# Kernel tuning notes

Hardware: AMD Instinct MI355X
Metric: run time of the kernel (lower is better)

The kernel has to match this reference:

```python
import jax, jax.numpy as jnp
import numpy as np

N, E, DIN, H, HEADS = 50000, 800000, 128, 64, 4


def setup_inputs() -> dict:
    key = jax.random.key(0)
    ks = jax.random.split(key, 12)

    def p(k, shape, fan_in):
        return jax.random.normal(k, shape, dtype=jnp.float32) / np.float32(np.sqrt(fan_in))

    return dict(
        x=jax.random.normal(ks[0], (N, DIN), dtype=jnp.float32),
        edge_index=jax.random.randint(ks[1], (2, E), 0, N, dtype=jnp.int32),
        # GCNConv(input_dim, hidden)
        W_gcn=p(ks[2], (DIN, H), DIN), b_gcn=jnp.zeros((H,), jnp.float32),
        # GATConv(hidden, hidden, heads=4, concat=True)
        W_gat=p(ks[3], (H, HEADS * H), H),
        att_src=p(ks[4], (HEADS, H), H), att_dst=p(ks[5], (HEADS, H), H),
        b_gat=jnp.zeros((HEADS * H,), jnp.float32),
        # SAGEConv(4*hidden, hidden): lin_l (neighbors, with bias), lin_r (root, no bias)
        W_sage_l=p(ks[6], (HEADS * H, H), HEADS * H), b_sage=jnp.zeros((H,), jnp.float32),
        W_sage_r=p(ks[7], (HEADS * H, H), HEADS * H),
        # edge-pair MLP: Linear(2*hidden, hidden) -> ReLU -> Linear(hidden, 1)
        W1=p(ks[8], (2 * H, H), 2 * H), b1=jnp.zeros((H,), jnp.float32),
        W2=p(ks[9], (H, 1), H), b2=jnp.zeros((1,), jnp.float32),
    )


def reference(x, edge_index, W_gcn, b_gcn, W_gat, att_src, att_dst, b_gat,
              W_sage_l, b_sage, W_sage_r, W1, b1, W2, b2):
    n = x.shape[0]
    src, dst = edge_index[0], edge_index[1]
    loop = jnp.arange(n, dtype=edge_index.dtype)
    # edges with self-loops appended (GCN and GAT add self-loops by default)
    s2 = jnp.concatenate([src, loop])
    d2 = jnp.concatenate([dst, loop])

    h = x @ W_gcn                                            # [N, H]
    deg = jax.ops.segment_sum(jnp.ones_like(d2, jnp.float32), d2, num_segments=n)
    dinv = jnp.where(deg > 0, jax.lax.rsqrt(jnp.maximum(deg, 1e-12)), 0.0)
    norm = dinv[s2] * dinv[d2]                               # [E+N]
    h = jax.ops.segment_sum(h[s2] * norm[:, None], d2, num_segments=n) + b_gcn
    h = jax.nn.relu(h)                                       # dropout: identity in eval

    # ---- GATConv (heads=4, concat=True, negative_slope=0.2) ----
    g = (h @ W_gat).reshape(n, HEADS, H)                     # [N, heads, C]
    a_s = jnp.sum(g * att_src, axis=-1)                      # [N, heads]
    a_d = jnp.sum(g * att_dst, axis=-1)
    e = jax.nn.leaky_relu(a_s[s2] + a_d[d2], 0.2)            # [E+N, heads]
    m = jax.ops.segment_max(e, d2, num_segments=n)           # per-target max (stable softmax)
    e = jnp.exp(e - m[d2])
    z = jax.ops.segment_sum(e, d2, num_segments=n)
    alpha = e / (z[d2] + 1e-16)                              # edge softmax over incoming edges
    g = jax.ops.segment_sum(g[s2] * alpha[:, :, None], d2, num_segments=n)
    g = jax.nn.relu(g.reshape(n, HEADS * H) + b_gat)

    # ---- SAGEConv (mean aggregation, root weight, no self-loops) ----
    nsum = jax.ops.segment_sum(g[src], dst, num_segments=n)
    cnt = jax.ops.segment_sum(jnp.ones_like(dst, jnp.float32), dst, num_segments=n)
    mean = nsum / jnp.maximum(cnt, 1.0)[:, None]
    s = jax.nn.relu(mean @ W_sage_l + b_sage + g @ W_sage_r)  # [N, H]

    # ---- edge-pair MLP + sigmoid ----
    ef = jnp.concatenate([s[src], s[dst]], axis=1)            # [E, 2H]
    pred = jax.nn.relu(ef @ W1 + b1) @ W2 + b2                # [E, 1]
    return jax.nn.sigmoid(pred[:, 0])
```

## Files before the change

kernel.cpp:

```cpp
#include <hip/hip_runtime.h>
#include <math.h>

typedef float v2f __attribute__((ext_vector_type(2)));
static __device__ __forceinline__ float4 f4s(float v){ return make_float4(v,v,v,v); }
static __device__ __forceinline__ float4 f4add(float4 a, float4 b){ return make_float4(a.x+b.x,a.y+b.y,a.z+b.z,a.w+b.w); }
static __device__ __forceinline__ float4 f4max(float4 a, float4 b){ return make_float4(fmaxf(a.x,b.x),fmaxf(a.y,b.y),fmaxf(a.z,b.z),fmaxf(a.w,b.w)); }
static __device__ __forceinline__ float4 f4scale(float4 a, float s){ return make_float4(a.x*s,a.y*s,a.z*s,a.w*s); }
static __device__ __forceinline__ float4 f4fma(float4 acc, float s, float4 b){
  acc.x += s*b.x; acc.y += s*b.y; acc.z += s*b.z; acc.w += s*b.w; return acc;
}
static __device__ __forceinline__ float4 f4relu(float4 a){ return f4max(a, f4s(0.f)); }
static __device__ __forceinline__ float4 f4leaky(float4 a){
  return make_float4(a.x>0.f?a.x:0.2f*a.x, a.y>0.f?a.y:0.2f*a.y, a.z>0.f?a.z:0.2f*a.z, a.w>0.f?a.w:0.2f*a.w);
}
static __device__ __forceinline__ float4 f4expf(float4 a){ return make_float4(__expf(a.x),__expf(a.y),__expf(a.z),__expf(a.w)); }
static __device__ __forceinline__ unsigned short f2bf(float f){
  unsigned int u = __float_as_uint(f);
  unsigned int r = (u + 0x7fffu + ((u >> 16) & 1u)) >> 16;
  return (unsigned short)r;
}
static __device__ __forceinline__ ushort4 f2bf4(float4 f){
  ushort4 r; r.x=f2bf(f.x); r.y=f2bf(f.y); r.z=f2bf(f.z); r.w=f2bf(f.w); return r;
}
static __device__ __forceinline__ float4 bfu2f4(uint2 u){
  return make_float4(__uint_as_float(u.x << 16), __uint_as_float(u.x & 0xffff0000u),
                     __uint_as_float(u.y << 16), __uint_as_float(u.y & 0xffff0000u));
}
static __device__ __forceinline__ float4 bfu2f4_lo(uint4 u){ return bfu2f4(make_uint2(u.x, u.y)); }
static __device__ __forceinline__ float4 bfu2f4_hi(uint4 u){ return bfu2f4(make_uint2(u.z, u.w)); }

typedef __attribute__((ext_vector_type(8))) unsigned short u16x8;
static __device__ __forceinline__ u16x8 f2bf8(float4 a, float4 b){
  u16x8 r;
  r[0]=f2bf(a.x); r[1]=f2bf(a.y); r[2]=f2bf(a.z); r[3]=f2bf(a.w);
  r[4]=f2bf(b.x); r[5]=f2bf(b.y); r[6]=f2bf(b.z); r[7]=f2bf(b.w);
  return r;
}
static __device__ __forceinline__ void red2(float4& a, float4& b){
  a.x += __shfl_xor(a.x, 8); a.y += __shfl_xor(a.y, 8);
  a.z += __shfl_xor(a.z, 8); a.w += __shfl_xor(a.w, 8);
  b.x += __shfl_xor(b.x, 8); b.y += __shfl_xor(b.y, 8);
  b.z += __shfl_xor(b.z, 8); b.w += __shfl_xor(b.w, 8);
}
static __device__ __forceinline__ unsigned char f2fp8(float v){
  return (unsigned char)(__builtin_amdgcn_cvt_pk_fp8_f32(v, v, 0, false) & 0xff);
}
static __device__ __forceinline__ unsigned int f4_fp8x4(float4 v){
  unsigned int r = __builtin_amdgcn_cvt_pk_fp8_f32(v.x, v.y, 0, false);
  r = __builtin_amdgcn_cvt_pk_fp8_f32(v.z, v.w, r, true);
  return r;
}
static __device__ __forceinline__ float4 fp8x4_f4(unsigned int q){
  v2f lo = __builtin_amdgcn_cvt_pk_f32_fp8(q, false);
  v2f hi = __builtin_amdgcn_cvt_pk_f32_fp8(q, true);
  return make_float4(lo[0], lo[1], hi[0], hi[1]);
}
static __device__ __forceinline__ float dot8(float4 a, float4 b, const float* v){
  return a.x*v[0]+a.y*v[1]+a.z*v[2]+a.w*v[3]+b.x*v[4]+b.y*v[5]+b.z*v[6]+b.w*v[7];
}

typedef __attribute__((ext_vector_type(8))) short bf16x8;
typedef __attribute__((ext_vector_type(4))) float f32x4;

__global__ __launch_bounds__(256) void k_rank(const int* __restrict__ dst, int* __restrict__ cnt,
                                              int* __restrict__ rank, int E){
  int t = blockIdx.x*256 + threadIdx.x;
  if (t < E) rank[t] = atomicAdd(&cnt[dst[t]], 1);
}
__global__ __launch_bounds__(256) void k_scan1(const int* __restrict__ cnt, int* __restrict__ excl,
                                               int* __restrict__ bsum, int n){
  __shared__ int sc[256];
  int t = threadIdx.x; int i = blockIdx.x*256 + t;
  int v = (i<n)?cnt[i]:0;
  sc[t]=v; __syncthreads();
  for (int o=1;o<256;o<<=1){ int a=(t>=o)?sc[t-o]:0; __syncthreads(); sc[t]+=a; __syncthreads(); }
  if (i<n) excl[i] = sc[t]-v;
  if (t==255) bsum[blockIdx.x] = sc[t];
}
__global__ __launch_bounds__(256) void k_scan2v(int* __restrict__ bsum, int nb,
                                                const float* __restrict__ Wg, const float* __restrict__ as,
                                                const float* __restrict__ ad, float* __restrict__ Vs,
                                                float* __restrict__ Vd){
  __shared__ int sc[256];
  int t = threadIdx.x;
  int v = (t<nb)?bsum[t]:0;
  sc[t]=v; __syncthreads();
  for (int o=1;o<256;o<<=1){ int a=(t>=o)?sc[t-o]:0; __syncthreads(); sc[t]+=a; __syncthreads(); }
  if (t<nb) bsum[t] = sc[t]-v;
  int h = t >> 6, k = t & 63;
  float s = 0.f, d = 0.f;
  const float* wr = Wg + (size_t)k*256 + h*64;
  const float* ar = as + h*64;
  const float* dr = ad + h*64;
  for (int c = 0; c < 64; ++c){ float w = wr[c]; s += w*ar[c]; d += w*dr[c]; }
  Vs[t] = s; Vd[t] = d;
}
__global__ __launch_bounds__(256) void k_scan3(const int* __restrict__ cnt, const int* __restrict__ excl,
                                               const int* __restrict__ bsum, int* __restrict__ offs,
                                               float* __restrict__ dinv, int n, int E){
  int i = blockIdx.x*256 + threadIdx.x;
  if (i < n){
    int o = excl[i] + bsum[blockIdx.x];
    offs[i] = o;
    dinv[i] = rsqrtf((float)cnt[i] + 1.0f);
    if (i == 0) offs[n] = E;
  }
}
__global__ __launch_bounds__(256) void k_fill(const int* __restrict__ src, const int* __restrict__ dst,
                                              const int* __restrict__ offs, const int* __restrict__ rank,
                                              int* __restrict__ csr, int E){
  int t = blockIdx.x*256 + threadIdx.x;
  if (t < E) csr[offs[dst[t]] + rank[t]] = src[t];
}

template<int K, int Cout, bool IBF16, bool SCALE, bool DUAL, bool H4, bool BRELU, bool OB16, bool O8>
__global__ __launch_bounds__(256) void k_mgemm(const void* __restrict__ in, int ldin,
                                               const float* __restrict__ Wa, int ldwa,
                                               const float* __restrict__ Wb, int ldwb,
                                               unsigned short* __restrict__ out,
                                               unsigned char* __restrict__ out8, int ldout,
                                               int n, const float* __restrict__ rowscale,
                                               const float* __restrict__ bias){
  constexpr int CC = Cout >> 4;
  constexpr int KB = K >> 5;
  constexpr int NH = H4 ? 4 : 1;
  extern __shared__ unsigned short wb[];
  int tid = threadIdx.x;
  constexpr int nslots = KB*CC*64;
  for (int s = tid; s < nslots; s += 256){
    int l = s & 63;
    int f = s >> 6;
    int cc = f % CC, kb = f / CC;
    int c  = cc*16 + (l & 15);
    int kr = kb*32 + ((l >> 4) << 3);
    const float* wp; int ld;
    if (DUAL && c >= (Cout/2)){ wp = Wb + (size_t)kr*ldwb + (c - Cout/2); ld = ldwb; }
    else                      { wp = Wa + (size_t)kr*ldwa + c;            ld = ldwa; }
    unsigned short* dp = &wb[s*8];
    #pragma unroll
    for (int j = 0; j < 8; ++j) dp[j] = f2bf(wp[(size_t)j*ld]);
  }
  __syncthreads();
  int wv = tid >> 6, l = tid & 63;
  int lrow = l & 15;
  int lk = (l >> 4) << 3;
  int ngrp = (n + 63) >> 6;
  const unsigned short* inb = (const unsigned short*)in;
  const float* inf = (const float*)in;
  for (int g = blockIdx.x; g < ngrp; g += gridDim.x){
    int r0 = (g << 6) + (wv << 4);
    int m = r0 + lrow;
    bf16x8 afr[NH][KB];
    #pragma unroll
    for (int h = 0; h < NH; ++h){
      #pragma unroll
      for (int kb = 0; kb < KB; ++kb){
        bf16x8 a = {0,0,0,0,0,0,0,0};
        if (m < n){
          int off = (H4 ? h*64 : 0) + kb*32 + lk;
          if (IBF16){
            a = *(const bf16x8*)(inb + (size_t)m*ldin + off);
          } else {
            const float* p = inf + (size_t)m*ldin + off;
            float4 f0 = *(const float4*)p;
            float4 f1 = *(const float4*)(p + 4);
            a[0]=(short)f2bf(f0.x); a[1]=(short)f2bf(f0.y); a[2]=(short)f2bf(f0.z); a[3]=(short)f2bf(f0.w);
            a[4]=(short)f2bf(f1.x); a[5]=(short)f2bf(f1.y); a[6]=(short)f2bf(f1.z); a[7]=(short)f2bf(f1.w);
          }
        }
        afr[h][kb] = a;
      }
    }
    int rbase = r0 + ((l >> 4) << 2);
    float sc[4];
    if (SCALE){
      #pragma unroll
      for (int r = 0; r < 4; ++r) sc[r] = (rbase + r < n) ? rowscale[rbase + r] : 0.f;
    }
    #pragma unroll
    for (int cc = 0; cc < CC; ++cc){
      f32x4 acc = {0.f, 0.f, 0.f, 0.f};
      constexpr int hstep = H4 ? 1 : 0;
      int hh = hstep ? (cc >> 2) : 0;
      #pragma unroll
      for (int kb = 0; kb < KB; ++kb){
        bf16x8 b = *(const bf16x8*)&wb[((kb*CC + cc)*64 + l)*8];
        acc = __builtin_amdgcn_mfma_f32_16x16x32_bf16(afr[hh][kb], b, acc, 0, 0, 0);
      }
      int c = cc*16 + lrow;
      float bv = BRELU ? bias[c] : 0.f;
      #pragma unroll
      for (int r = 0; r < 4; ++r){
        int rr = rbase + r;
        if (rr < n){
          float v = acc[r];
          if (SCALE) v *= sc[r];
          if (BRELU) v = fmaxf(v + bv, 0.f);
          if (OB16) out[(size_t)rr*ldout + c] = f2bf(v);
          if (O8)   out8[(size_t)rr*ldout + c] = f2fp8(v);
        }
      }
    }
  }
}

__global__ __launch_bounds__(256) void k_gatsage(const unsigned short* __restrict__ Y,
                                                 const float* __restrict__ Wg,
                                                 const float* __restrict__ bg,
                                                 const float* __restrict__ Wl,
                                                 const float* __restrict__ Wr,
                                                 unsigned short* __restrict__ R,
                                                 unsigned char* __restrict__ P8, int n){
  constexpr int LDG = 264;
  extern __shared__ unsigned short lds[];
  unsigned short* wb1 = lds;
  unsigned short* wb2 = wb1 + 2048*8;
  unsigned short* gb  = wb2 + 4096*8;
  int tid = threadIdx.x;
  for (int s = tid; s < 2048; s += 256){
    int l = s & 63, f = s >> 6;
    int cc = f & 15, kb = f >> 4;
    int c  = cc*16 + (l & 15);
    int kr = kb*32 + ((l >> 4) << 3);
    const float* wp = Wg + (size_t)kr*256 + c;
    unsigned short* dp = &wb1[s*8];
    #pragma unroll
    for (int j = 0; j < 8; ++j) dp[j] = f2bf(wp[(size_t)j*256]);
  }
  for (int s = tid; s < 4096; s += 256){
    int l = s & 63, f = s >> 6;
    int cc = f & 7, kb = f >> 3;
    int c  = cc*16 + (l & 15);
    int kr = kb*32 + ((l >> 4) << 3);
    const float* wp = (c >= 64) ? (Wr + (size_t)kr*64 + (c - 64)) : (Wl + (size_t)kr*64 + c);
    unsigned short* dp = &wb2[s*8];
    #pragma unroll
    for (int j = 0; j < 8; ++j) dp[j] = f2bf(wp[(size_t)j*64]);
  }
  __syncthreads();
  int wv = tid >> 6, l = tid & 63;
  int lrow = l & 15;
  int lk = (l >> 4) << 3;
  int rbase4 = (l >> 4) << 2;
  int ngrp = (n + 63) >> 6;
  for (int g = blockIdx.x; g < ngrp; g += gridDim.x){
    int r0 = (g << 6) + (wv << 4);
    int m = r0 + lrow;
    bf16x8 afr[4][2];
    #pragma unroll
    for (int h = 0; h < 4; ++h){
      #pragma unroll
      for (int kb = 0; kb < 2; ++kb){
        bf16x8 a = {0,0,0,0,0,0,0,0};
        if (m < n) a = *(const bf16x8*)(Y + (size_t)m*256 + h*64 + kb*32 + lk);
        afr[h][kb] = a;
      }
    }
    #pragma unroll
    for (int cc = 0; cc < 16; ++cc){
      f32x4 acc = {0.f, 0.f, 0.f, 0.f};
      int hh = cc >> 2;
      #pragma unroll
      for (int kb = 0; kb < 2; ++kb){
        bf16x8 b = *(const bf16x8*)&wb1[((kb*16 + cc)*64 + l)*8];
        acc = __builtin_amdgcn_mfma_f32_16x16x32_bf16(afr[hh][kb], b, acc, 0, 0, 0);
      }
      int c = cc*16 + lrow;
      float bv = bg[c];
      #pragma unroll
      for (int r = 0; r < 4; ++r){
        int lr = (wv << 4) + rbase4 + r;
        gb[lr*LDG + c] = f2bf(fmaxf(acc[r] + bv, 0.f));
      }
    }
    bf16x8 afb[8];
    #pragma unroll
    for (int kb = 0; kb < 8; ++kb)
      afb[kb] = *(const bf16x8*)&gb[((wv << 4) + lrow)*LDG + kb*32 + lk];
    #pragma unroll
    for (int cc = 0; cc < 8; ++cc){
      f32x4 acc = {0.f, 0.f, 0.f, 0.f};
      #pragma unroll
      for (int kb = 0; kb < 8; ++kb){
        bf16x8 b = *(const bf16x8*)&wb2[((kb*8 + cc)*64 + l)*8];
        acc = __builtin_amdgcn_mfma_f32_16x16x32_bf16(afb[kb], b, acc, 0, 0, 0);
      }
      int c = cc*16 + lrow;
      #pragma unroll
      for (int r = 0; r < 4; ++r){
        int rr = r0 + rbase4 + r;
        if (rr < n){
          float v = acc[r];
          if (c < 64) P8[(size_t)rr*64 + c] = f2fp8(v);
          else        R[(size_t)rr*64 + (c - 64)] = f2bf(v);
        }
      }
    }
  }
}

__global__ __launch_bounds__(256) void k_gcn(const unsigned char* __restrict__ a8, const float* __restrict__ dinv,
                                             const float* __restrict__ b, const int* __restrict__ offs,
                                             const int* __restrict__ csr, const float* __restrict__ Vs,
                                             const float* __restrict__ Vd, unsigned char* __restrict__ h8,
                                             float* __restrict__ D, int n){
  __shared__ float svs[256], svd[256];
  svs[threadIdx.x] = Vs[threadIdx.x];
  svd[threadIdx.x] = Vd[threadIdx.x];
  __syncthreads();
  int l = threadIdx.x & 63;
  int node = (((blockIdx.x*256 + threadIdx.x) >> 6) << 2) + (l >> 4);
  int l15 = l & 15;
  int grp = l15 >> 3, sub = l15 & 7;
  bool ok = node < n;
  int beg = 0, end = 0;
  float di = 0.f;
  if (ok){ beg = offs[node]; end = offs[node+1]; di = dinv[node]; }
  float4 aL0 = f4s(0.f), aH0 = f4s(0.f), aL1 = f4s(0.f), aH1 = f4s(0.f);
  int i = beg + grp;
  for (; i + 2 < end; i += 4){
    int s0 = csr[i], s1 = csr[i+2];
    uint2 u0 = *(const uint2*)(a8 + (size_t)s0*64 + (sub<<3));
    uint2 u1 = *(const uint2*)(a8 + (size_t)s1*64 + (sub<<3));
    aL0 = f4add(aL0, fp8x4_f4(u0.x)); aH0 = f4add(aH0, fp8x4_f4(u0.y));
    aL1 = f4add(aL1, fp8x4_f4(u1.x)); aH1 = f4add(aH1, fp8x4_f4(u1.y));
  }
  if (i < end){
    int s0 = csr[i];
    uint2 u0 = *(const uint2*)(a8 + (size_t)s0*64 + (sub<<3));
    aL0 = f4add(aL0, fp8x4_f4(u0.x)); aH0 = f4add(aH0, fp8x4_f4(u0.y));
  }
  float4 aL = f4add(aL0, aL1), aH = f4add(aH0, aH1);
  red2(aL, aH);
  if (ok){
    uint2 us = *(const uint2*)(a8 + (size_t)node*64 + (sub<<3));
    aL = f4add(aL, fp8x4_f4(us.x)); aH = f4add(aH, fp8x4_f4(us.y));
    float4 b0 = *(const float4*)(b + (sub<<3));
    float4 b1 = *(const float4*)(b + (sub<<3) + 4);
    float4 r0 = f4relu(f4fma(b0, di, aL));
    float4 r1 = f4relu(f4fma(b1, di, aH));
    if (grp == 0){
      uint2 q; q.x = f4_fp8x4(r0); q.y = f4_fp8x4(r1);
      *(uint2*)(h8 + (size_t)node*64 + (sub<<3)) = q;
    }
    const float* vs0 = svs + (grp*128) + (sub<<3);
    const float* vd0 = svd + (grp*128) + (sub<<3);
    float s0 = dot8(r0, r1, vs0);
    float s1 = dot8(r0, r1, vs0 + 64);
    float d0 = dot8(r0, r1, vd0);
    float d1 = dot8(r0, r1, vd0 + 64);
    #pragma unroll
    for (int o = 1; o < 8; o <<= 1){
      s0 += __shfl_xor(s0, o); s1 += __shfl_xor(s1, o);
      d0 += __shfl_xor(d0, o); d1 += __shfl_xor(d1, o);
    }
    if (sub == 0){
      *(float2*)(D + (size_t)node*8 + grp*2)     = make_float2(s0, s1);
      *(float2*)(D + (size_t)node*8 + 4 + grp*2) = make_float2(d0, d1);
    }
  }
}

#define GAT_CAP 128
__global__ __launch_bounds__(256) void k_gat2(const float* __restrict__ D, const unsigned char* __restrict__ H8,
                                              const int* __restrict__ offs, const int* __restrict__ csr,
                                              unsigned short* __restrict__ Y, int n){
  __shared__ float wl[8][GAT_CAP*4];
  __shared__ int   sl[8][GAT_CAP];
  int hw = threadIdx.x >> 5;
  int node = (blockIdx.x*256 + threadIdx.x) >> 5;
  int l5 = threadIdx.x & 31;
  if (node >= n) return;
  int beg = offs[node], end = offs[node+1];
  int deg = end - beg;
  float4 ed  = *(const float4*)(D + (size_t)node*8 + 4);
  float4 es0 = *(const float4*)(D + (size_t)node*8);
  float4 wself = f4expf(f4leaky(f4add(es0, ed)));
  float4 z4 = f4s(0.f);
  for (int i = beg + l5; i < end; i += 32){
    int s = csr[i];
    float4 w = f4expf(f4leaky(f4add(*(const float4*)(D + (size_t)s*8), ed)));
    int li = i - beg;
    if (li < GAT_CAP){ *(float4*)&wl[hw][li<<2] = w; sl[hw][li] = s << 6; }
    z4 = f4add(z4, w);
  }
  for (int m = 1; m < 32; m <<= 1){
    z4.x += __shfl_xor(z4.x, m); z4.y += __shfl_xor(z4.y, m);
    z4.z += __shfl_xor(z4.z, m); z4.w += __shfl_xor(z4.w, m);
  }
  z4 = f4add(z4, wself);
  int grp = l5 >> 4;
  int sub = l5 & 15;
  int c0b = sub << 2;
  float4 a0 = f4s(0.f), a1 = f4s(0.f), a2 = f4s(0.f), a3 = f4s(0.f);
  int nl = deg < GAT_CAP ? deg : GAT_CAP;
  int i = grp;
  for (; i + 2 < nl; i += 4){
    int o0 = sl[hw][i], o1 = sl[hw][i+2];
    float4 w0 = *(const float4*)&wl[hw][i<<2];
    float4 w1 = *(const float4*)&wl[hw][(i+2)<<2];
    unsigned int q0 = *(const unsigned int*)(H8 + o0 + c0b);
    unsigned int q1 = *(const unsigned int*)(H8 + o1 + c0b);
    float4 f0 = fp8x4_f4(q0);
    float4 f1 = fp8x4_f4(q1);
    a0 = f4fma(a0, w0.x, f0); a1 = f4fma(a1, w0.y, f0);
    a2 = f4fma(a2, w0.z, f0); a3 = f4fma(a3, w0.w, f0);
    a0 = f4fma(a0, w1.x, f1); a1 = f4fma(a1, w1.y, f1);
    a2 = f4fma(a2, w1.z, f1); a3 = f4fma(a3, w1.w, f1);
  }
  if (i < nl){
    float4 w0 = *(const float4*)&wl[hw][i<<2];
    float4 f0 = fp8x4_f4(*(const unsigned int*)(H8 + sl[hw][i] + c0b));
    a0 = f4fma(a0, w0.x, f0); a1 = f4fma(a1, w0.y, f0);
    a2 = f4fma(a2, w0.z, f0); a3 = f4fma(a3, w0.w, f0);
  }
  for (int j = nl + grp; j < deg; j += 2){
    int s = csr[beg+j];
    float4 e = f4leaky(f4add(*(const float4*)(D + (size_t)s*8), ed));
    float4 w = f4expf(e);
    float4 f0 = fp8x4_f4(*(const unsigned int*)(H8 + ((size_t)s << 6) + c0b));
    a0 = f4fma(a0, w.x, f0); a1 = f4fma(a1, w.y, f0);
    a2 = f4fma(a2, w.z, f0); a3 = f4fma(a3, w.w, f0);
  }
  a0.x += __shfl_xor(a0.x, 16); a0.y += __shfl_xor(a0.y, 16); a0.z += __shfl_xor(a0.z, 16); a0.w += __shfl_xor(a0.w, 16);
  a1.x += __shfl_xor(a1.x, 16); a1.y += __shfl_xor(a1.y, 16); a1.z += __shfl_xor(a1.z, 16); a1.w += __shfl_xor(a1.w, 16);
  a2.x += __shfl_xor(a2.x, 16); a2.y += __shfl_xor(a2.y, 16); a2.z += __shfl_xor(a2.z, 16); a2.w += __shfl_xor(a2.w, 16);
  a3.x += __shfl_xor(a3.x, 16); a3.y += __shfl_xor(a3.y, 16); a3.z += __shfl_xor(a3.z, 16); a3.w += __shfl_xor(a3.w, 16);
  if (grp == 0){
    float4 fs = fp8x4_f4(*(const unsigned int*)(H8 + ((size_t)node << 6) + c0b));
    a0 = f4fma(a0, wself.x, fs);
    a1 = f4fma(a1, wself.y, fs);
    a2 = f4fma(a2, wself.z, fs);
    a3 = f4fma(a3, wself.w, fs);
    a0 = f4scale(a0, 1.f/(z4.x + 1e-16f));
    a1 = f4scale(a1, 1.f/(z4.y + 1e-16f));
    a2 = f4scale(a2, 1.f/(z4.z + 1e-16f));
    a3 = f4scale(a3, 1.f/(z4.w + 1e-16f));
    unsigned short* yp = Y + (size_t)node*256 + (sub << 2);
    *(ushort4*)(yp)       = f2bf4(a0);
    *(ushort4*)(yp + 64)  = f2bf4(a1);
    *(ushort4*)(yp + 128) = f2bf4(a2);
    *(ushort4*)(yp + 192) = f2bf4(a3);
  }
}

__global__ __launch_bounds__(256) void k_sage(const unsigned char* __restrict__ P8, const unsigned short* __restrict__ R,
                                              const float* __restrict__ b, const int* __restrict__ offs,
                                              const int* __restrict__ csr, unsigned short* __restrict__ S, int n){
  int l = threadIdx.x & 63;
  int node = (((blockIdx.x*256 + threadIdx.x) >> 6) << 2) + (l >> 4);
  int l15 = l & 15;
  int grp = l15 >> 3, sub = l15 & 7;
  bool ok = node < n;
  int beg = 0, end = 0;
  if (ok){ beg = offs[node]; end = offs[node+1]; }
  float4 aL0 = f4s(0.f), aH0 = f4s(0.f), aL1 = f4s(0.f), aH1 = f4s(0.f);
  int i = beg + grp;
  for (; i + 2 < end; i += 4){
    int s0 = csr[i], s1 = csr[i+2];
    uint2 u0 = *(const uint2*)(P8 + (size_t)s0*64 + (sub<<3));
    uint2 u1 = *(const uint2*)(P8 + (size_t)s1*64 + (sub<<3));
    aL0 = f4add(aL0, fp8x4_f4(u0.x)); aH0 = f4add(aH0, fp8x4_f4(u0.y));
    aL1 = f4add(aL1, fp8x4_f4(u1.x)); aH1 = f4add(aH1, fp8x4_f4(u1.y));
  }
  if (i < end){
    int s0 = csr[i];
    uint2 u0 = *(const uint2*)(P8 + (size_t)s0*64 + (sub<<3));
    aL0 = f4add(aL0, fp8x4_f4(u0.x)); aH0 = f4add(aH0, fp8x4_f4(u0.y));
  }
  float4 aL = f4add(aL0, aL1), aH = f4add(aH0, aH1);
  red2(aL, aH);
  if (ok && grp == 0){
    float minv = 1.f / fmaxf((float)(end - beg), 1.f);
    uint4 ur = *(const uint4*)(R + (size_t)node*64 + (sub<<3));
    float4 b0 = *(const float4*)(b + (sub<<3));
    float4 b1 = *(const float4*)(b + (sub<<3) + 4);
    float4 r0 = f4relu(f4add(f4fma(b0, minv, aL), bfu2f4_lo(ur)));
    float4 r1 = f4relu(f4add(f4fma(b1, minv, aH), bfu2f4_hi(ur)));
    *(u16x8*)(S + (size_t)node*64 + (sub<<3)) = f2bf8(r0, r1);
  }
}

__global__ __launch_bounds__(256) void k_mlp(const unsigned char* __restrict__ T2,
                                             const float* __restrict__ b1, const float* __restrict__ W2,
                                             const float* __restrict__ b2, const int* __restrict__ src,
                                             const int* __restrict__ dst, float* __restrict__ out, int E){
  int t = threadIdx.x;
  int e = blockIdx.x*32 + (t >> 3);
  if (e >= E) return;
  int sub = t & 7;
  int s = src[e], d = dst[e];
  uint2 uu = *(const uint2*)(T2 + (size_t)s*128 + (sub<<3));
  uint2 vv = *(const uint2*)(T2 + (size_t)d*128 + 64 + (sub<<3));
  float4 u0 = fp8x4_f4(uu.x), u1 = fp8x4_f4(uu.y);
  float4 v0 = fp8x4_f4(vv.x), v1 = fp8x4_f4(vv.y);
  float4 bb0 = *(const float4*)(b1 + (sub<<3));
  float4 bb1 = *(const float4*)(b1 + (sub<<3) + 4);
  float4 w0 = *(const float4*)(W2 + (sub<<3));
  float4 w1 = *(const float4*)(W2 + (sub<<3) + 4);
  float4 ta = f4relu(f4add(f4add(u0, v0), bb0));
  float4 tb = f4relu(f4add(f4add(u1, v1), bb1));
  float p = ta.x*w0.x + ta.y*w0.y + ta.z*w0.z + ta.w*w0.w
          + tb.x*w1.x + tb.y*w1.y + tb.z*w1.z + tb.w*w1.w;
  p += __shfl_xor(p, 1);
  p += __shfl_xor(p, 2);
  p += __shfl_xor(p, 4);
  if (sub == 0) out[e] = 1.f / (1.f + __expf(-(p + b2[0])));
}

extern "C" void kernel_launch(void* const* d_in, const int* in_sizes, int n_in,
                              void* d_out, int out_size, void* d_ws, size_t ws_size,
                              hipStream_t stream){
  const float* x     = (const float*)d_in[0];
  const int*   eidx  = (const int*)  d_in[1];
  const float* W_gcn = (const float*)d_in[2];
  const float* b_gcn = (const float*)d_in[3];
  const float* W_gat = (const float*)d_in[4];
  const float* att_s = (const float*)d_in[5];
  const float* att_d = (const float*)d_in[6];
  const float* b_gat = (const float*)d_in[7];
  const float* W_sl  = (const float*)d_in[8];
  const float* b_sg  = (const float*)d_in[9];
  const float* W_sr  = (const float*)d_in[10];
  const float* W1    = (const float*)d_in[11];
  const float* b1    = (const float*)d_in[12];
  const float* W2    = (const float*)d_in[13];
  const float* b2    = (const float*)d_in[14];
  float* out = (float*)d_out;

  const int N = in_sizes[0] / 128;
  const int E = in_sizes[1] / 2;
  const int* src = eidx;
  const int* dst = eidx + E;

  float* ws   = (float*)d_ws;
  float* dinv = ws;
  float* D    = dinv + (size_t)N;
  float* Vs   = D + (size_t)N*8;
  float* Vd   = Vs + 256;
  unsigned short* Y  = (unsigned short*)(Vd + 256);
  unsigned short* R  = Y + (size_t)N*256;
  unsigned short* S  = R + (size_t)N*64;
  unsigned char*  A8 = (unsigned char*)(S + (size_t)N*64);
  unsigned char*  H8 = A8 + (size_t)N*64;
  unsigned char*  P8 = H8 + (size_t)N*64;
  unsigned char*  T2 = P8 + (size_t)N*64;
  int* cnt  = (int*)(T2 + (size_t)N*128);
  int* excl = cnt + N;
  int* bsum = excl + N;
  int* offs = bsum + 256;
  int* rank = offs + N + 1;
  int* csr  = rank + E;

  const int nb = (N + 255) / 256;
  const int gtiles = (N + 63) / 64;
  const int nwb = (N + 15) / 16;
  const int GSH = (2048*8 + 4096*8 + 64*264) * 2;

  static bool s_attr = false;
  if (!s_attr){
    hipFuncSetAttribute((const void*)k_gatsage, hipFuncAttributeMaxDynamicSharedMemorySize, GSH);
    s_attr = true;
  }

  hipMemsetAsync(cnt, 0, (size_t)N*sizeof(int), stream);
  k_rank<<<(E+255)/256, 256, 0, stream>>>(dst, cnt, rank, E);
  k_scan1<<<nb, 256, 0, stream>>>(cnt, excl, bsum, N);
  k_scan2v<<<1, 256, 0, stream>>>(bsum, nb, W_gat, att_s, att_d, Vs, Vd);
  k_scan3<<<nb, 256, 0, stream>>>(cnt, excl, bsum, offs, dinv, N, E);
  k_fill<<<(E+255)/256, 256, 0, stream>>>(src, dst, offs, rank, csr, E);

  k_mgemm<128, 64, false, true, false, false, false, false, true><<<gtiles, 256, 128*64*2, stream>>>(
      x, 128, W_gcn, 64, nullptr, 0, nullptr, A8, 64, N, dinv, nullptr);
  k_gcn <<<nwb, 256, 0, stream>>>(A8, dinv, b_gcn, offs, csr, Vs, Vd, H8, D, N);

  k_gat2<<<(N+7)/8, 256, 0, stream>>>(D, H8, offs, csr, Y, N);

  k_gatsage<<<256, 256, GSH, stream>>>(Y, W_gat, b_gat, W_sl, W_sr, R, P8, N);

  k_sage<<<nwb, 256, 0, stream>>>(P8, R, b_sg, offs, csr, S, N);

  k_mgemm<64, 128, true, false, true, false, false, false, true><<<gtiles, 256, 64*128*2, stream>>>(
      S, 64, W1, 64, W1 + 64*64, 64, nullptr, T2, 128, N, nullptr, nullptr);
  k_mlp <<<(E+31)/32, 256, 0, stream>>>(T2, b1, W2, b2, src, dst, out, E);
}
```

Before: 291.0 us.

## Process edge MLP per destination node via CSR with edge-id permutation

```diff
diff --git a/kernel.cpp b/kernel.cpp
--- a/kernel.cpp
+++ b/kernel.cpp
@@ -108,17 +108,22 @@
 }
 __global__ __launch_bounds__(256) void k_fill(const int* __restrict__ src, const int* __restrict__ dst,
                                               const int* __restrict__ offs, const int* __restrict__ rank,
-                                              int* __restrict__ csr, int E){
+                                              int* __restrict__ csr, int* __restrict__ eidv, int E){
   int t = blockIdx.x*256 + threadIdx.x;
-  if (t < E) csr[offs[dst[t]] + rank[t]] = src[t];
-}
-
-template<int K, int Cout, bool IBF16, bool SCALE, bool DUAL, bool H4, bool BRELU, bool OB16, bool O8>
+  if (t < E){
+    int pos = offs[dst[t]] + rank[t];
+    csr[pos]  = src[t];
+    eidv[pos] = t;
+  }
+}
+
+template<int K, int Cout, bool IBF16, bool SCALE, bool DUAL, bool H4, bool BRELU, bool OB16, bool O8, bool SPL>
 __global__ __launch_bounds__(256) void k_mgemm(const void* __restrict__ in, int ldin,
                                                const float* __restrict__ Wa, int ldwa,
                                                const float* __restrict__ Wb, int ldwb,
                                                unsigned short* __restrict__ out,
-                                               unsigned char* __restrict__ out8, int ldout,
+                                               unsigned char* __restrict__ out8,
+                                               unsigned char* __restrict__ out8b, int ldout,
                                                int n, const float* __restrict__ rowscale,
                                                const float* __restrict__ bias){
   constexpr int CC = Cout >> 4;
@@ -197,7 +202,14 @@
           if (SCALE) v *= sc[r];
           if (BRELU) v = fmaxf(v + bv, 0.f);
           if (OB16) out[(size_t)rr*ldout + c] = f2bf(v);
-          if (O8)   out8[(size_t)rr*ldout + c] = f2fp8(v);
+          if (O8){
+            if (SPL){
+              if (c < (Cout >> 1)) out8 [(size_t)rr*ldout + c] = f2fp8(v);
+              else                 out8b[(size_t)rr*ldout + (c - (Cout >> 1))] = f2fp8(v);
+            } else {
+              out8[(size_t)rr*ldout + c] = f2fp8(v);
+            }
+          }
         }
       }
     }
@@ -481,31 +493,39 @@
   }
 }
 
-__global__ __launch_bounds__(256) void k_mlp(const unsigned char* __restrict__ T2,
+__global__ __launch_bounds__(256) void k_mlp(const unsigned char* __restrict__ U8,
+                                             const unsigned char* __restrict__ V8,
                                              const float* __restrict__ b1, const float* __restrict__ W2,
-                                             const float* __restrict__ b2, const int* __restrict__ src,
-                                             const int* __restrict__ dst, float* __restrict__ out, int E){
-  int t = threadIdx.x;
-  int e = blockIdx.x*32 + (t >> 3);
-  if (e >= E) return;
-  int sub = t & 7;
-  int s = src[e], d = dst[e];
-  uint2 uu = *(const uint2*)(T2 + (size_t)s*128 + (sub<<3));
-  uint2 vv = *(const uint2*)(T2 + (size_t)d*128 + 64 + (sub<<3));
-  float4 u0 = fp8x4_f4(uu.x), u1 = fp8x4_f4(uu.y);
-  float4 v0 = fp8x4_f4(vv.x), v1 = fp8x4_f4(vv.y);
+                                             const float* __restrict__ b2, const int* __restrict__ offs,
+                                             const int* __restrict__ csr, const int* __restrict__ eid,
+                                             float* __restrict__ out, int n){
+  int l5 = threadIdx.x & 31;
+  int node = (blockIdx.x*256 + threadIdx.x) >> 5;
+  if (node >= n) return;
+  int beg = offs[node], end = offs[node+1];
+  if (beg == end) return;
+  int sub  = l5 & 7;
+  int slot = l5 >> 3;
+  uint2 vv = *(const uint2*)(V8 + (size_t)node*64 + (sub<<3));
   float4 bb0 = *(const float4*)(b1 + (sub<<3));
   float4 bb1 = *(const float4*)(b1 + (sub<<3) + 4);
+  float4 v0 = f4add(fp8x4_f4(vv.x), bb0);
+  float4 v1 = f4add(fp8x4_f4(vv.y), bb1);
   float4 w0 = *(const float4*)(W2 + (sub<<3));
   float4 w1 = *(const float4*)(W2 + (sub<<3) + 4);
-  float4 ta = f4relu(f4add(f4add(u0, v0), bb0));
-  float4 tb = f4relu(f4add(f4add(u1, v1), bb1));
-  float p = ta.x*w0.x + ta.y*w0.y + ta.z*w0.z + ta.w*w0.w
-          + tb.x*w1.x + tb.y*w1.y + tb.z*w1.z + tb.w*w1.w;
-  p += __shfl_xor(p, 1);
-  p += __shfl_xor(p, 2);
-  p += __shfl_xor(p, 4);
-  if (sub == 0) out[e] = 1.f / (1.f + __expf(-(p + b2[0])));
+  float b2v = b2[0];
+  for (int i = beg + slot; i < end; i += 4){
+    int s = csr[i];
+    uint2 uu = *(const uint2*)(U8 + (size_t)s*64 + (sub<<3));
+    float4 ta = f4relu(f4add(fp8x4_f4(uu.x), v0));
+    float4 tb = f4relu(f4add(fp8x4_f4(uu.y), v1));
+    float p = ta.x*w0.x + ta.y*w0.y + ta.z*w0.z + ta.w*w0.w
+            + tb.x*w1.x + tb.y*w1.y + tb.z*w1.z + tb.w*w1.w;
+    p += __shfl_xor(p, 1);
+    p += __shfl_xor(p, 2);
+    p += __shfl_xor(p, 4);
+    if (sub == 0) out[eid[i]] = 1.f / (1.f + __expf(-(p + b2v)));
+  }
 }
 
 extern "C" void kernel_launch(void* const* d_in, const int* in_sizes, int n_in,
@@ -544,13 +564,15 @@
   unsigned char*  A8 = (unsigned char*)(S + (size_t)N*64);
   unsigned char*  H8 = A8 + (size_t)N*64;
   unsigned char*  P8 = H8 + (size_t)N*64;
-  unsigned char*  T2 = P8 + (size_t)N*64;
-  int* cnt  = (int*)(T2 + (size_t)N*128);
+  unsigned char*  U8 = P8 + (size_t)N*64;
+  unsigned char*  V8 = U8 + (size_t)N*64;
+  int* cnt  = (int*)(V8 + (size_t)N*64);
   int* excl = cnt + N;
   int* bsum = excl + N;
   int* offs = bsum + 256;
   int* rank = offs + N + 1;
   int* csr  = rank + E;
+  int* eid  = csr + E;
 
   const int nb = (N + 255) / 256;
   const int gtiles = (N + 63) / 64;
@@ -568,10 +590,10 @@
   k_scan1<<<nb, 256, 0, stream>>>(cnt, excl, bsum, N);
   k_scan2v<<<1, 256, 0, stream>>>(bsum, nb, W_gat, att_s, att_d, Vs, Vd);
   k_scan3<<<nb, 256, 0, stream>>>(cnt, excl, bsum, offs, dinv, N, E);
-  k_fill<<<(E+255)/256, 256, 0, stream>>>(src, dst, offs, rank, csr, E);
-
-  k_mgemm<128, 64, false, true, false, false, false, false, true><<<gtiles, 256, 128*64*2, stream>>>(
-      x, 128, W_gcn, 64, nullptr, 0, nullptr, A8, 64, N, dinv, nullptr);
+  k_fill<<<(E+255)/256, 256, 0, stream>>>(src, dst, offs, rank, csr, eid, E);
+
+  k_mgemm<128, 64, false, true, false, false, false, false, true, false><<<gtiles, 256, 128*64*2, stream>>>(
+      x, 128, W_gcn, 64, nullptr, 0, nullptr, A8, nullptr, 64, N, dinv, nullptr);
   k_gcn <<<nwb, 256, 0, stream>>>(A8, dinv, b_gcn, offs, csr, Vs, Vd, H8, D, N);
 
   k_gat2<<<(N+7)/8, 256, 0, stream>>>(D, H8, offs, csr, Y, N);
@@ -580,7 +602,7 @@
 
   k_sage<<<nwb, 256, 0, stream>>>(P8, R, b_sg, offs, csr, S, N);
 
-  k_mgemm<64, 128, true, false, true, false, false, false, true><<<gtiles, 256, 64*128*2, stream>>>(
-      S, 64, W1, 64, W1 + 64*64, 64, nullptr, T2, 128, N, nullptr, nullptr);
-  k_mlp <<<(E+31)/32, 256, 0, stream>>>(T2, b1, W2, b2, src, dst, out, E);
-}
+  k_mgemm<64, 128, true, false, true, false, false, false, true, true><<<gtiles, 256, 64*128*2, stream>>>(
+      S, 64, W1, 64, W1 + 64*64, 64, nullptr, U8, V8, 64, N, nullptr, nullptr);
+  k_mlp <<<(N+7)/8, 256, 0, stream>>>(U8, V8, b1, W2, b2, offs, csr, eid, out, N);
+}
```

New measurement: 307.0 us. +5.5%, slower.

## Fuse SAGE aggregation with edge-MLP first-layer projection GEMM via MFMA

Applied to the files above, without the earlier changes.

```diff
diff --git a/kernel.cpp b/kernel.cpp
--- a/kernel.cpp
+++ b/kernel.cpp
@@ -446,9 +446,25 @@
 
 __global__ __launch_bounds__(256) void k_sage(const unsigned char* __restrict__ P8, const unsigned short* __restrict__ R,
                                               const float* __restrict__ b, const int* __restrict__ offs,
-                                              const int* __restrict__ csr, unsigned short* __restrict__ S, int n){
-  int l = threadIdx.x & 63;
-  int node = (((blockIdx.x*256 + threadIdx.x) >> 6) << 2) + (l >> 4);
+                                              const int* __restrict__ csr, const float* __restrict__ W1a,
+                                              const float* __restrict__ W1b, unsigned char* __restrict__ T2, int n){
+  __shared__ unsigned short wfr[1024*8];
+  __shared__ unsigned short stile[16][72];
+  int tid = threadIdx.x;
+  for (int s = tid; s < 1024; s += 256){
+    int l = s & 63, f = s >> 6;
+    int cc = f & 7, kb = f >> 3;
+    int c  = cc*16 + (l & 15);
+    int kr = kb*32 + ((l >> 4) << 3);
+    const float* wp = (c >= 64) ? (W1b + (size_t)kr*64 + (c - 64)) : (W1a + (size_t)kr*64 + c);
+    unsigned short* dp = &wfr[s*8];
+    #pragma unroll
+    for (int j = 0; j < 8; ++j) dp[j] = f2bf(wp[(size_t)j*64]);
+  }
+  int wv = tid >> 6, l = tid & 63;
+  int base = blockIdx.x*16;
+  int lrow16 = (wv << 2) + (l >> 4);
+  int node = base + lrow16;
   int l15 = l & 15;
   int grp = l15 >> 3, sub = l15 & 7;
   bool ok = node < n;
@@ -470,14 +486,33 @@
   }
   float4 aL = f4add(aL0, aL1), aH = f4add(aH0, aH1);
   red2(aL, aH);
-  if (ok && grp == 0){
+  float4 r0 = f4s(0.f), r1 = f4s(0.f);
+  if (ok){
     float minv = 1.f / fmaxf((float)(end - beg), 1.f);
     uint4 ur = *(const uint4*)(R + (size_t)node*64 + (sub<<3));
     float4 b0 = *(const float4*)(b + (sub<<3));
     float4 b1 = *(const float4*)(b + (sub<<3) + 4);
-    float4 r0 = f4relu(f4add(f4fma(b0, minv, aL), bfu2f4_lo(ur)));
-    float4 r1 = f4relu(f4add(f4fma(b1, minv, aH), bfu2f4_hi(ur)));
-    *(u16x8*)(S + (size_t)node*64 + (sub<<3)) = f2bf8(r0, r1);
+    r0 = f4relu(f4add(f4fma(b0, minv, aL), bfu2f4_lo(ur)));
+    r1 = f4relu(f4add(f4fma(b1, minv, aH), bfu2f4_hi(ur)));
+  }
+  if (grp == 0) *(u16x8*)&stile[lrow16][sub << 3] = f2bf8(r0, r1);
+  __syncthreads();
+  int lrow = l & 15, lk = (l >> 4) << 3;
+  bf16x8 af0 = *(const bf16x8*)&stile[lrow][lk];
+  bf16x8 af1 = *(const bf16x8*)&stile[lrow][32 + lk];
+  int rbase = (l >> 4) << 2;
+  #pragma unroll
+  for (int q = 0; q < 2; ++q){
+    int cc = wv*2 + q;
+    f32x4 acc = {0.f, 0.f, 0.f, 0.f};
+    acc = __builtin_amdgcn_mfma_f32_16x16x32_bf16(af0, *(const bf16x8*)&wfr[(cc*64 + l)*8], acc, 0, 0, 0);
+    acc = __builtin_amdgcn_mfma_f32_16x16x32_bf16(af1, *(const bf16x8*)&wfr[((8 + cc)*64 + l)*8], acc, 0, 0, 0);
+    int c = cc*16 + lrow;
+    #pragma unroll
+    for (int r = 0; r < 4; ++r){
+      int nd = base + rbase + r;
+      if (nd < n) T2[(size_t)nd*128 + c] = f2fp8(acc[r]);
+    }
   }
 }
 
@@ -540,8 +575,7 @@
   float* Vd   = Vs + 256;
   unsigned short* Y  = (unsigned short*)(Vd + 256);
   unsigned short* R  = Y + (size_t)N*256;
-  unsigned short* S  = R + (size_t)N*64;
-  unsigned char*  A8 = (unsigned char*)(S + (size_t)N*64);
+  unsigned char*  A8 = (unsigned char*)(R + (size_t)N*64);
   unsigned char*  H8 = A8 + (size_t)N*64;
   unsigned char*  P8 = H8 + (size_t)N*64;
   unsigned char*  T2 = P8 + (size_t)N*64;
@@ -578,9 +612,7 @@
 
   k_gatsage<<<256, 256, GSH, stream>>>(Y, W_gat, b_gat, W_sl, W_sr, R, P8, N);
 
-  k_sage<<<nwb, 256, 0, stream>>>(P8, R, b_sg, offs, csr, S, N);
-
-  k_mgemm<64, 128, true, false, true, false, false, false, true><<<gtiles, 256, 64*128*2, stream>>>(
-      S, 64, W1, 64, W1 + 64*64, 64, nullptr, T2, 128, N, nullptr, nullptr);
+  k_sage<<<nwb, 256, 0, stream>>>(P8, R, b_sg, offs, csr, W1, W1 + 64*64, T2, N);
+
   k_mlp <<<(E+31)/32, 256, 0, stream>>>(T2, b1, W2, b2, src, dst, out, E);
 }
```

New measurement: 290.5 us. About the same (-0.2%).
